# Optimization experiments

Hardware: AMD Instinct MI355X
Metric: run time of the kernel (lower is better)

## Reference

```python
import jax, jax.numpy as jnp
import numpy as np

B, N, C = 8, 1024, 1024
H = 16
D = C // H  # head_dim = 64


def apply_rope(t, cos, sin):
    # t: (B,H,N,D), cos/sin: (N, D//2). Interleaved-pair RoPE
    # (matches repeat_interleave(2) + stack(-y2,y1) in the torch code).
    tr = t.reshape(*t.shape[:-1], D // 2, 2)
    t1, t2 = tr[..., 0], tr[..., 1]
    o1 = t1 * cos - t2 * sin
    o2 = t2 * cos + t1 * sin
    return jnp.stack((o1, o2), axis=-1).reshape(t.shape)


def setup_inputs() -> dict:
    key = jax.random.key(0)
    k1, k2, k3, k4 = jax.random.split(key, 4)
    s = 0.02
    x = jax.random.normal(k1, (B, N, C), dtype=jnp.float32)
    w_qkv = jax.random.normal(k2, (C, 3 * C), dtype=jnp.float32) * s  # qkv_bias=False
    w_proj = jax.random.normal(k3, (C, C), dtype=jnp.float32) * s
    b_proj = jax.random.normal(k4, (C,), dtype=jnp.float32) * s
    return {"x": x, "w_qkv": w_qkv, "w_proj": w_proj, "b_proj": b_proj}


def reference(x, w_qkv, w_proj, b_proj):
    # QKV projection: (B,N,3C) -> (3,B,H,N,D)
    qkv = (x @ w_qkv).reshape(B, N, 3, H, D).transpose(2, 0, 3, 1, 4)
    q, k, v = qkv[0], qkv[1], qkv[2]

    # RoPE tables: pos = arange(N) (mask=None, no cls/registers)
    pos = jnp.arange(N, dtype=jnp.float32)
    omega = 1.0 / (10000.0 ** (jnp.arange(D // 2, dtype=jnp.float32) / (D / 2.0)))
    freq = pos[:, None] * omega  # (N, D//2)
    cos, sin = jnp.cos(freq), jnp.sin(freq)

    q = apply_rope(q, cos, sin)
    k = apply_rope(k, cos, sin)

    # Scaled dot-product attention (non-causal, no dropout in eval)
    scale = 1.0 / jnp.sqrt(jnp.float32(D))
    scores = jnp.einsum('bhqd,bhkd->bhqk', q, k) * scale
    attn = jax.nn.softmax(scores, axis=-1)
    out = jnp.einsum('bhqk,bhkd->bhqd', attn, v)

    # Merge heads + output projection
    out = out.transpose(0, 2, 1, 3).reshape(B, N, C)
    return out @ w_proj + b_proj
```

## Files before the change

kernel.cpp:

```cpp
#include <hip/hip_runtime.h>
#include <hip/hip_bf16.h>
#include <math.h>

#define Bsz  8
#define Nseq 1024
#define Cdim 1024
#define Hh   16
#define Dd   64

typedef short short8 __attribute__((ext_vector_type(8)));
typedef float floatx4 __attribute__((ext_vector_type(4)));

__device__ __forceinline__ unsigned short f2bf(float f) {
    __hip_bfloat16 h = __float2bfloat16(f);
    return __builtin_bit_cast(unsigned short, h);
}

__device__ __forceinline__ void async16(const void* g, void* l) {
    __builtin_amdgcn_global_load_lds(
        (const __attribute__((address_space(1))) unsigned int*)g,
        (__attribute__((address_space(3))) unsigned int*)l, 16, 0, 0);
}

__device__ __forceinline__ unsigned pack_bf16(float lo, float hi) {
    unsigned ulo = __float_as_uint(lo) + 0x8000u;
    unsigned uhi = __float_as_uint(hi) + 0x8000u;
    return __builtin_amdgcn_perm(uhi, ulo, 0x07060302);
}

__device__ __forceinline__ float exp2_raw(float x) {
    float r;
    asm("v_exp_f32 %0, %1" : "=v"(r) : "v"(x));
    return r;
}

__global__ __launch_bounds__(256) void prep(
    const float* __restrict__ x, const float* __restrict__ w_qkv,
    const float* __restrict__ w_proj,
    unsigned short* __restrict__ xb, unsigned short* __restrict__ wqkvt,
    unsigned short* __restrict__ wprojt, float2* __restrict__ rope)
{
    __shared__ float T[64][65];
    const int blk = blockIdx.x;
    const int tid = threadIdx.x;

    if (blk < 8192) {
        int i = blk * 256 + tid;
        float4 v = ((const float4*)x)[i];
        ushort4 u;
        u.x = f2bf(v.x); u.y = f2bf(v.y); u.z = f2bf(v.z); u.w = f2bf(v.w);
        ((ushort4*)xb)[i] = u;
        return;
    }
    if (blk < 9216) {
        const float* in;
        unsigned short* out;
        int R = 1024, Ccols, c0, r0;
        if (blk < 8960) {
            int b2 = blk - 8192;
            in = w_qkv; out = wqkvt; Ccols = 3072;
            c0 = (b2 % 48) * 64; r0 = (b2 / 48) * 64;
        } else {
            int b2 = blk - 8960;
            in = w_proj; out = wprojt; Ccols = 1024;
            c0 = (b2 % 16) * 64; r0 = (b2 / 16) * 64;
        }
        for (int i = tid; i < 4096; i += 256) {
            int r = i >> 6, c = i & 63;
            T[r][c] = in[(size_t)(r0 + r) * Ccols + c0 + c];
        }
        __syncthreads();
        for (int i = tid; i < 4096; i += 256) {
            int rr = i >> 6, cc = i & 63;
            out[(size_t)(c0 + rr) * R + r0 + cc] = f2bf(T[cc][rr]);
        }
        return;
    }
    {
        int i = (blk - 9216) * 256 + tid;
        int n = i >> 5, p = i & 31;
        float omega = __expf(-(float)p * 0.2878231366242557f);
        float sv, cv;
        sincosf((float)n * omega, &sv, &cv);
        rope[i] = make_float2(cv, sv);
    }
}

__global__ __launch_bounds__(256, 2) void gemm_qkv(
    const unsigned short* __restrict__ A, const unsigned short* __restrict__ Bt,
    const float2* __restrict__ rope,
    unsigned short* __restrict__ qb, unsigned short* __restrict__ kb,
    unsigned short* __restrict__ vtb)
{
    __shared__ __attribute__((aligned(16))) short SM[32768];
    const int tid  = threadIdx.x;
    const int wave = tid >> 6, lane = tid & 63;
    const int ml = lane & 15, quad = lane >> 4;
    const int wm = wave >> 1, wn = wave & 1;

    int lin = blockIdx.y * 8 + blockIdx.x;
    lin = (lin & 7) * 64 + (lin >> 3);
    const int bm = (lin >> 3) * 128;
    const int bn = (lin & 7) * 128;

    const int lr     = lane >> 3;
    const int lchunk = ((lane & 7) ^ lr) * 8;

    floatx4 acc[3][4][4] = {};

    for (int k0 = 0; k0 < 1024; k0 += 64) {
        #pragma unroll
        for (int t = 0; t < 4; ++t) {
            int r8 = (wave * 4 + t) * 8;
            async16(A + (size_t)(bm + r8 + lr) * 1024 + k0 + lchunk, &SM[r8 * 64]);
        }
        #pragma unroll
        for (int rg = 0; rg < 3; ++rg)
            #pragma unroll
            for (int t = 0; t < 4; ++t) {
                int r8 = (wave * 4 + t) * 8;
                async16(Bt + (size_t)(rg * 1024 + bn + r8 + lr) * 1024 + k0 + lchunk,
                        &SM[8192 + rg * 8192 + r8 * 64]);
            }
        __syncthreads();

        #pragma unroll
        for (int ks = 0; ks < 2; ++ks) {
            const int sl = ((ks * 4 + quad) ^ (ml & 7)) * 8;
            short8 araw[4];
            #pragma unroll
            for (int mi = 0; mi < 4; ++mi)
                araw[mi] = *(const short8*)&SM[(wm * 64 + mi * 16 + ml) * 64 + sl];
            #pragma unroll
            for (int rg = 0; rg < 3; ++rg) {
                short8 braw[4];
                #pragma unroll
                for (int ni = 0; ni < 4; ++ni)
                    braw[ni] = *(const short8*)&SM[8192 + rg * 8192 +
                                                   (wn * 64 + ni * 16 + ml) * 64 + sl];
                #pragma unroll
                for (int mi = 0; mi < 4; ++mi)
                    #pragma unroll
                    for (int ni = 0; ni < 4; ++ni)
                        acc[rg][mi][ni] = __builtin_amdgcn_mfma_f32_16x16x32_bf16(
                            araw[mi], braw[ni], acc[rg][mi][ni], 0, 0, 0);
            }
        }
        __syncthreads();
    }

    const int b  = bm >> 10;
    const int n0 = bm & 1023;

    float2* Rs = (float2*)SM;
    #pragma unroll
    for (int t = 0; t < 16; ++t) {
        int idx = t * 256 + tid;
        Rs[idx] = rope[(size_t)(n0 + (idx >> 5)) * 32 + (idx & 31)];
    }
    __syncthreads();

    #pragma unroll
    for (int rg = 0; rg < 2; ++rg) {
        unsigned short* dst = (rg == 0) ? qb : kb;
        const float scale = (rg == 0) ? 0.1803368801111602f : 1.f;
        const float sgn = (ml & 1) ? 1.f : -1.f;
        #pragma unroll
        for (int ni = 0; ni < 4; ++ni) {
            int jj = bn + wn * 64 + ni * 16 + ml;
            int h = jj >> 6, d = jj & 63, p = d >> 1;
            #pragma unroll
            for (int mi = 0; mi < 4; ++mi)
                #pragma unroll
                for (int r = 0; r < 4; ++r) {
                    int rl = wm * 64 + mi * 16 + quad * 4 + r;
                    float val = acc[rg][mi][ni][r];
                    float partner = __shfl_xor(val, 1);
                    float2 cs = Rs[rl * 32 + p];
                    dst[(((size_t)(b * Hh + h)) * Nseq + n0 + rl) * Dd + d] =
                        f2bf((val * cs.x + sgn * partner * cs.y) * scale);
                }
        }
    }

    {
        short* T = SM + 16384;
        #pragma unroll
        for (int hw = 0; hw < 2; ++hw) {
            if (hw) __syncthreads();
            if (wn == hw) {
                #pragma unroll
                for (int ni = 0; ni < 4; ++ni) {
                    int dcol = ni * 16 + ml;
                    #pragma unroll
                    for (int mi = 0; mi < 4; ++mi)
                        #pragma unroll
                        for (int r = 0; r < 4; ++r) {
                            int rl = wm * 64 + mi * 16 + quad * 4 + r;
                            T[dcol * 132 + rl] = (short)f2bf(acc[2][mi][ni][r]);
                        }
                }
            }
            __syncthreads();
            int h = (bn >> 6) + hw;
            #pragma unroll
            for (int t = 0; t < 8; ++t) {
                int idx4 = t * 256 + tid;
                int d = idx4 >> 5, seg = idx4 & 31;
                ushort4 v4 = *(const ushort4*)&T[d * 132 + seg * 4];
                *(ushort4*)(vtb + (((size_t)(b * Hh + h)) * Dd + d) * Nseq
                            + n0 + seg * 4) = v4;
            }
        }
    }
}

__global__ __launch_bounds__(256) void gemm_proj(
    const unsigned short* __restrict__ A, const unsigned short* __restrict__ Bt,
    const float* __restrict__ bias, float* __restrict__ out)
{
    const int K = 1024;
    __shared__ short SM[2][128][64];
    const int tid  = threadIdx.x;
    const int wave = tid >> 6, lane = tid & 63;
    const int ml = lane & 15, quad = lane >> 4;
    const int wm = wave >> 1, wn = wave & 1;

    int lin = blockIdx.y * gridDim.x + blockIdx.x;
    const int nwg = gridDim.x * gridDim.y;
    lin = (lin & 7) * (nwg >> 3) + (lin >> 3);
    const int bx = lin % gridDim.x, by = lin / gridDim.x;
    const int bm = by * 128, bn = bx * 128;

    const int lr     = lane >> 3;
    const int lchunk = ((lane & 7) ^ lr) * 8;

    floatx4 acc[4][4] = {};

    for (int k0 = 0; k0 < K; k0 += 64) {
        #pragma unroll
        for (int t = 0; t < 4; ++t) {
            int r8  = (wave * 4 + t) * 8;
            int row = r8 + lr;
            async16(A  + (size_t)(bm + row) * K + k0 + lchunk, &SM[0][r8][0]);
            async16(Bt + (size_t)(bn + row) * K + k0 + lchunk, &SM[1][r8][0]);
        }
        __syncthreads();

        #pragma unroll
        for (int ks = 0; ks < 2; ++ks) {
            const int sl = ((ks * 4 + quad) ^ (ml & 7)) * 8;
            short8 araw[4], braw[4];
            #pragma unroll
            for (int mi = 0; mi < 4; ++mi)
                araw[mi] = *(const short8*)&SM[0][wm * 64 + mi * 16 + ml][sl];
            #pragma unroll
            for (int ni = 0; ni < 4; ++ni)
                braw[ni] = *(const short8*)&SM[1][wn * 64 + ni * 16 + ml][sl];
            #pragma unroll
            for (int mi = 0; mi < 4; ++mi)
                #pragma unroll
                for (int ni = 0; ni < 4; ++ni)
                    acc[mi][ni] = __builtin_amdgcn_mfma_f32_16x16x32_bf16(
                        araw[mi], braw[ni], acc[mi][ni], 0, 0, 0);
        }
        __syncthreads();
    }

    #pragma unroll
    for (int ni = 0; ni < 4; ++ni) {
        int col = bn + wn * 64 + ni * 16 + ml;
        float bv = bias[col];
        #pragma unroll
        for (int mi = 0; mi < 4; ++mi)
            #pragma unroll
            for (int r = 0; r < 4; ++r) {
                int row = bm + wm * 64 + mi * 16 + quad * 4 + r;
                out[(size_t)row * 1024 + col] = acc[mi][ni][r] + bv;
            }
    }
}

__global__ __launch_bounds__(256, 4) void attn_flash_mfma(
    const unsigned short* __restrict__ qb, const unsigned short* __restrict__ kb,
    const unsigned short* __restrict__ vt, unsigned short* __restrict__ ao)
{
    const int bh  = blockIdx.x;
    const int qt  = blockIdx.y;
    const int tid = threadIdx.x;
    const int wave = tid >> 6, lane = tid & 63;
    const int ml = lane & 15, quad = lane >> 4;
    const int lr = lane >> 3;
    const int lc = ((lane & 7) ^ lr) * 8;

    __shared__ __attribute__((aligned(16))) short SMEM[17408];
    short (*Ks)[64] = (short(*)[64])SMEM;
    short* U = SMEM + 4096;
    short (*Qs)[64] = (short(*)[64])U;
    short (*Vs)[64] = (short(*)[64])U;
    short (*Ps)[32][72] = (short(*)[32][72])(U + 4096);

    const size_t hbase = (size_t)bh * (Nseq * Dd);
    const size_t vbase = (size_t)bh * 64;
    const int q0 = qt * 128;
    const int wq = wave * 32;
    const int wk = wave * 16;

    #pragma unroll
    for (int t = 0; t < 4; ++t)
        async16(qb + hbase + (size_t)(q0 + wq + t * 8 + lr) * 64 + lc, &Qs[wq + t * 8][0]);
    async16(kb + hbase + (size_t)(wk + lr) * 64 + lc,     &Ks[wk][0]);
    async16(kb + hbase + (size_t)(wk + 8 + lr) * 64 + lc, &Ks[wk + 8][0]);
    __syncthreads();

    short8 qfr[2][2];
    #pragma unroll
    for (int ks = 0; ks < 2; ++ks) {
        const int sl = ((ks * 4 + quad) ^ (ml & 7)) * 8;
        qfr[ks][0] = *(const short8*)&Qs[wq + ml][sl];
        qfr[ks][1] = *(const short8*)&Qs[wq + 16 + ml][sl];
    }
    __syncthreads();

    float l0 = 0.f, l1 = 0.f;
    floatx4 o[2][4] = {};

    for (int kt = 0; kt < 16; ++kt) {
        const int k0r = kt * 64;
        async16(vt + (vbase + wk + lr) * Nseq + k0r + lc,     &Vs[wk][0]);
        async16(vt + (vbase + wk + 8 + lr) * Nseq + k0r + lc, &Vs[wk + 8][0]);

        floatx4 st[2][4] = {};
        __builtin_amdgcn_s_setprio(1);
        #pragma unroll
        for (int ks = 0; ks < 2; ++ks) {
            const int sl = ((ks * 4 + quad) ^ (ml & 7)) * 8;
            #pragma unroll
            for (int kbk = 0; kbk < 4; ++kbk) {
                short8 kf = *(const short8*)&Ks[kbk * 16 + ml][sl];
                st[0][kbk] = __builtin_amdgcn_mfma_f32_16x16x32_bf16(kf, qfr[ks][0], st[0][kbk], 0, 0, 0);
                st[1][kbk] = __builtin_amdgcn_mfma_f32_16x16x32_bf16(kf, qfr[ks][1], st[1][kbk], 0, 0, 0);
            }
        }
        __builtin_amdgcn_s_setprio(0);

        #pragma unroll
        for (int qg = 0; qg < 2; ++qg) {
            float lacc = 0.f;
            #pragma unroll
            for (int kbk = 0; kbk < 4; ++kbk) {
                float e0 = exp2_raw(st[qg][kbk][0]);
                float e1 = exp2_raw(st[qg][kbk][1]);
                float e2 = exp2_raw(st[qg][kbk][2]);
                float e3 = exp2_raw(st[qg][kbk][3]);
                lacc += (e0 + e1) + (e2 + e3);
                uint2 pk;
                pk.x = pack_bf16(e0, e1);
                pk.y = pack_bf16(e2, e3);
                *(uint2*)&Ps[wave][qg * 16 + ml][kbk * 16 + quad * 4] = pk;
            }
            if (qg == 0) l0 += lacc; else l1 += lacc;
        }
        __syncthreads();

        if (kt < 15) {
            const int k1r = k0r + 64;
            async16(kb + hbase + (size_t)(k1r + wk + lr) * 64 + lc,     &Ks[wk][0]);
            async16(kb + hbase + (size_t)(k1r + wk + 8 + lr) * 64 + lc, &Ks[wk + 8][0]);
        }

        __builtin_amdgcn_s_setprio(1);
        #pragma unroll
        for (int ks = 0; ks < 2; ++ks) {
            const int sl = ((ks * 4 + quad) ^ (ml & 7)) * 8;
            short8 pf0 = *(const short8*)&Ps[wave][ml][ks * 32 + quad * 8];
            short8 pf1 = *(const short8*)&Ps[wave][16 + ml][ks * 32 + quad * 8];
            #pragma unroll
            for (int nt = 0; nt < 4; ++nt) {
                short8 vf = *(const short8*)&Vs[nt * 16 + ml][sl];
                o[0][nt] = __builtin_amdgcn_mfma_f32_16x16x32_bf16(pf0, vf, o[0][nt], 0, 0, 0);
                o[1][nt] = __builtin_amdgcn_mfma_f32_16x16x32_bf16(pf1, vf, o[1][nt], 0, 0, 0);
            }
        }
        __builtin_amdgcn_s_setprio(0);
        if (kt < 15)
            __syncthreads();
    }

    l0 += __shfl_xor(l0, 16);
    l0 += __shfl_xor(l0, 32);
    l1 += __shfl_xor(l1, 16);
    l1 += __shfl_xor(l1, 32);

    const int b = bh >> 4, h = bh & 15;
    #pragma unroll
    for (int qg = 0; qg < 2; ++qg) {
        float lsrc = (qg == 0) ? l0 : l1;
        #pragma unroll
        for (int r = 0; r < 4; ++r) {
            float lq = __shfl(lsrc, quad * 4 + r);
            float inv = 1.f / lq;
            int q = q0 + wq + qg * 16 + quad * 4 + r;
            size_t rowbase = ((size_t)(b * Nseq + q)) * Cdim + h * Dd;
            #pragma unroll
            for (int nt = 0; nt < 4; ++nt)
                ao[rowbase + nt * 16 + ml] = f2bf(o[qg][nt][r] * inv);
        }
    }
}

extern "C" void kernel_launch(void* const* d_in, const int* in_sizes, int n_in,
                              void* d_out, int out_size, void* d_ws, size_t ws_size,
                              hipStream_t stream) {
    const float* x      = (const float*)d_in[0];
    const float* w_qkv  = (const float*)d_in[1];
    const float* w_proj = (const float*)d_in[2];
    const float* b_proj = (const float*)d_in[3];
    float* out = (float*)d_out;

    const size_t M8 = (size_t)8 * 1024 * 1024;
    unsigned short* qb     = (unsigned short*)d_ws;
    unsigned short* kb     = qb + M8;
    unsigned short* vt     = kb + M8;
    unsigned short* xb     = vt + M8;
    unsigned short* wqkvt  = xb + M8;
    unsigned short* wprojt = wqkvt + 3 * 1024 * 1024;
    float2*         rope   = (float2*)(wprojt + 1024 * 1024);
    unsigned short* aob    = xb;

    prep<<<9344, 256, 0, stream>>>(x, w_qkv, w_proj, xb, wqkvt, wprojt, rope);

    gemm_qkv<<<dim3(8, 64), 256, 0, stream>>>(xb, wqkvt, rope, qb, kb, vt);

    attn_flash_mfma<<<dim3(128, 8), 256, 0, stream>>>(qb, kb, vt, aob);

    gemm_proj<<<dim3(8, 64), 256, 0, stream>>>(aob, wprojt, b_proj, out);
}
```

Baseline: 246.7 us.

## Retile QKV GEMM to 128x256 blocks per region and use hardware bf16 pack

The QKV GEMM no longer computes a 128x128 tile across all three Q/K/V regions at once. Each block now computes a 128x256 tile within a single region, with each wave covering all 128 rows and 64 columns. The grid grows to 12x64, LDS shrinks to 24576 shorts, and launch bounds allow 3 blocks per CU, aiming for better occupancy and wave balance. A native v_cvt_pk_bf16_f32 replaces manual rounding in the attention P packing and the V transpose, which changes rounding from round-half-up to the instruction's own rounding.

```diff
diff --git a/kernel.cpp b/kernel.cpp
--- a/kernel.cpp
+++ b/kernel.cpp
@@ -22,10 +22,10 @@
         (__attribute__((address_space(3))) unsigned int*)l, 16, 0, 0);
 }
 
-__device__ __forceinline__ unsigned pack_bf16(float lo, float hi) {
-    unsigned ulo = __float_as_uint(lo) + 0x8000u;
-    unsigned uhi = __float_as_uint(hi) + 0x8000u;
-    return __builtin_amdgcn_perm(uhi, ulo, 0x07060302);
+__device__ __forceinline__ unsigned cvt_pk_bf16(float lo, float hi) {
+    unsigned r;
+    asm("v_cvt_pk_bf16_f32 %0, %1, %2" : "=v"(r) : "v"(lo), "v"(hi));
+    return r;
 }
 
 __device__ __forceinline__ float exp2_raw(float x) {
@@ -86,27 +86,26 @@
     }
 }
 
-__global__ __launch_bounds__(256, 2) void gemm_qkv(
+__global__ __launch_bounds__(256, 3) void gemm_qkv(
     const unsigned short* __restrict__ A, const unsigned short* __restrict__ Bt,
     const float2* __restrict__ rope,
     unsigned short* __restrict__ qb, unsigned short* __restrict__ kb,
     unsigned short* __restrict__ vtb)
 {
-    __shared__ __attribute__((aligned(16))) short SM[32768];
+    __shared__ __attribute__((aligned(16))) short SM[24576];
     const int tid  = threadIdx.x;
     const int wave = tid >> 6, lane = tid & 63;
     const int ml = lane & 15, quad = lane >> 4;
-    const int wm = wave >> 1, wn = wave & 1;
-
-    int lin = blockIdx.y * 8 + blockIdx.x;
-    lin = (lin & 7) * 64 + (lin >> 3);
-    const int bm = (lin >> 3) * 128;
-    const int bn = (lin & 7) * 128;
+    const int wn = wave;
+
+    int lin = blockIdx.y * 12 + blockIdx.x;
+    lin = (lin & 7) * 96 + (lin >> 3);
+    const int bm = (lin / 12) * 128, bn = (lin % 12) * 256;
 
     const int lr     = lane >> 3;
     const int lchunk = ((lane & 7) ^ lr) * 8;
 
-    floatx4 acc[3][4][4] = {};
+    floatx4 acc[8][4] = {};
 
     for (int k0 = 0; k0 < 1024; k0 += 64) {
         #pragma unroll
@@ -115,99 +114,95 @@
             async16(A + (size_t)(bm + r8 + lr) * 1024 + k0 + lchunk, &SM[r8 * 64]);
         }
         #pragma unroll
-        for (int rg = 0; rg < 3; ++rg)
-            #pragma unroll
-            for (int t = 0; t < 4; ++t) {
-                int r8 = (wave * 4 + t) * 8;
-                async16(Bt + (size_t)(rg * 1024 + bn + r8 + lr) * 1024 + k0 + lchunk,
-                        &SM[8192 + rg * 8192 + r8 * 64]);
-            }
+        for (int t = 0; t < 8; ++t) {
+            int r8 = (wave * 8 + t) * 8;
+            async16(Bt + (size_t)(bn + r8 + lr) * 1024 + k0 + lchunk,
+                    &SM[8192 + r8 * 64]);
+        }
         __syncthreads();
 
         #pragma unroll
         for (int ks = 0; ks < 2; ++ks) {
             const int sl = ((ks * 4 + quad) ^ (ml & 7)) * 8;
-            short8 araw[4];
-            #pragma unroll
-            for (int mi = 0; mi < 4; ++mi)
-                araw[mi] = *(const short8*)&SM[(wm * 64 + mi * 16 + ml) * 64 + sl];
-            #pragma unroll
-            for (int rg = 0; rg < 3; ++rg) {
-                short8 braw[4];
+            short8 braw[4];
+            #pragma unroll
+            for (int ni = 0; ni < 4; ++ni)
+                braw[ni] = *(const short8*)&SM[8192 + (wn * 64 + ni * 16 + ml) * 64 + sl];
+            #pragma unroll
+            for (int mh = 0; mh < 2; ++mh) {
+                short8 araw[4];
                 #pragma unroll
-                for (int ni = 0; ni < 4; ++ni)
-                    braw[ni] = *(const short8*)&SM[8192 + rg * 8192 +
-                                                   (wn * 64 + ni * 16 + ml) * 64 + sl];
+                for (int mi = 0; mi < 4; ++mi)
+                    araw[mi] = *(const short8*)&SM[(mh * 64 + mi * 16 + ml) * 64 + sl];
                 #pragma unroll
                 for (int mi = 0; mi < 4; ++mi)
                     #pragma unroll
                     for (int ni = 0; ni < 4; ++ni)
-                        acc[rg][mi][ni] = __builtin_amdgcn_mfma_f32_16x16x32_bf16(
-                            araw[mi], braw[ni], acc[rg][mi][ni], 0, 0, 0);
-            }
-        }
-        __syncthreads();
-    }
-
+                        acc[mh * 4 + mi][ni] = __builtin_amdgcn_mfma_f32_16x16x32_bf16(
+                            araw[mi], braw[ni], acc[mh * 4 + mi][ni], 0, 0, 0);
+            }
+        }
+        __syncthreads();
+    }
+
+    const int region = bn >> 10;
     const int b  = bm >> 10;
     const int n0 = bm & 1023;
-
-    float2* Rs = (float2*)SM;
-    #pragma unroll
-    for (int t = 0; t < 16; ++t) {
-        int idx = t * 256 + tid;
-        Rs[idx] = rope[(size_t)(n0 + (idx >> 5)) * 32 + (idx & 31)];
-    }
-    __syncthreads();
-
-    #pragma unroll
-    for (int rg = 0; rg < 2; ++rg) {
-        unsigned short* dst = (rg == 0) ? qb : kb;
-        const float scale = (rg == 0) ? 0.1803368801111602f : 1.f;
+    if (region < 2) {
+        float2* Rs = (float2*)SM;
+        #pragma unroll
+        for (int t = 0; t < 16; ++t) {
+            int idx = t * 256 + tid;
+            Rs[idx] = rope[(size_t)(n0 + (idx >> 5)) * 32 + (idx & 31)];
+        }
+        __syncthreads();
+        unsigned short* dst = (region == 0) ? qb : kb;
+        const float scale = (region == 0) ? 0.1803368801111602f : 1.f;
         const float sgn = (ml & 1) ? 1.f : -1.f;
         #pragma unroll
         for (int ni = 0; ni < 4; ++ni) {
-            int jj = bn + wn * 64 + ni * 16 + ml;
+            int jj = (bn & 1023) + wn * 64 + ni * 16 + ml;
             int h = jj >> 6, d = jj & 63, p = d >> 1;
             #pragma unroll
-            for (int mi = 0; mi < 4; ++mi)
+            for (int mi = 0; mi < 8; ++mi)
                 #pragma unroll
                 for (int r = 0; r < 4; ++r) {
-                    int rl = wm * 64 + mi * 16 + quad * 4 + r;
-                    float val = acc[rg][mi][ni][r];
+                    int rl = mi * 16 + quad * 4 + r;
+                    float val = acc[mi][ni][r];
                     float partner = __shfl_xor(val, 1);
                     float2 cs = Rs[rl * 32 + p];
                     dst[(((size_t)(b * Hh + h)) * Nseq + n0 + rl) * Dd + d] =
                         f2bf((val * cs.x + sgn * partner * cs.y) * scale);
                 }
         }
-    }
-
-    {
-        short* T = SM + 16384;
-        #pragma unroll
-        for (int hw = 0; hw < 2; ++hw) {
-            if (hw) __syncthreads();
-            if (wn == hw) {
+    } else {
+        const int hb0 = (bn & 1023) >> 6;
+        #pragma unroll
+        for (int pp = 0; pp < 2; ++pp) {
+            if (pp) __syncthreads();
+            if ((wn >> 1) == pp) {
+                short* T = SM + (wn & 1) * 8448;
                 #pragma unroll
                 for (int ni = 0; ni < 4; ++ni) {
                     int dcol = ni * 16 + ml;
                     #pragma unroll
-                    for (int mi = 0; mi < 4; ++mi)
-                        #pragma unroll
-                        for (int r = 0; r < 4; ++r) {
-                            int rl = wm * 64 + mi * 16 + quad * 4 + r;
-                            T[dcol * 132 + rl] = (short)f2bf(acc[2][mi][ni][r]);
-                        }
+                    for (int mi = 0; mi < 8; ++mi) {
+                        uint2 pk;
+                        pk.x = cvt_pk_bf16(acc[mi][ni][0], acc[mi][ni][1]);
+                        pk.y = cvt_pk_bf16(acc[mi][ni][2], acc[mi][ni][3]);
+                        *(uint2*)&T[dcol * 132 + mi * 16 + quad * 4] = pk;
+                    }
                 }
             }
             __syncthreads();
-            int h = (bn >> 6) + hw;
-            #pragma unroll
-            for (int t = 0; t < 8; ++t) {
+            #pragma unroll
+            for (int t = 0; t < 16; ++t) {
                 int idx4 = t * 256 + tid;
-                int d = idx4 >> 5, seg = idx4 & 31;
-                ushort4 v4 = *(const ushort4*)&T[d * 132 + seg * 4];
+                int half = idx4 >> 11;
+                int rem  = idx4 & 2047;
+                int d = rem >> 5, seg = rem & 31;
+                ushort4 v4 = *(const ushort4*)&SM[half * 8448 + d * 132 + seg * 4];
+                int h = hb0 + pp * 2 + half;
                 *(ushort4*)(vtb + (((size_t)(b * Hh + h)) * Dd + d) * Nseq
                             + n0 + seg * 4) = v4;
             }
@@ -355,8 +350,8 @@
                 float e3 = exp2_raw(st[qg][kbk][3]);
                 lacc += (e0 + e1) + (e2 + e3);
                 uint2 pk;
-                pk.x = pack_bf16(e0, e1);
-                pk.y = pack_bf16(e2, e3);
+                pk.x = cvt_pk_bf16(e0, e1);
+                pk.y = cvt_pk_bf16(e2, e3);
                 *(uint2*)&Ps[wave][qg * 16 + ml][kbk * 16 + quad * 4] = pk;
             }
             if (qg == 0) l0 += lacc; else l1 += lacc;
@@ -430,7 +425,7 @@
 
     prep<<<9344, 256, 0, stream>>>(x, w_qkv, w_proj, xb, wqkvt, wprojt, rope);
 
-    gemm_qkv<<<dim3(8, 64), 256, 0, stream>>>(xb, wqkvt, rope, qb, kb, vt);
+    gemm_qkv<<<dim3(12, 64), 256, 0, stream>>>(xb, wqkvt, rope, qb, kb, vt);
 
     attn_flash_mfma<<<dim3(128, 8), 256, 0, stream>>>(qb, kb, vt, aob);
 
```

New measurement: 306.7 us. 1.24x slower.
